# Kernel tuning notes

Measured on AMD Instinct MI355X. Metric: run time of the kernel, lower is better.

The kernel has to match this reference:

```python
import jax, jax.numpy as jnp
import numpy as np

SIZES = [64, 64, 64, 64]
N_SAMPLES = 8192


def radialkernel(u, v):
    # exp(u.v^T - |u|^2/2 - |v|^2/2), shape [rows(u), rows(v)]
    uu = jnp.sum(u * u, axis=1, keepdims=True)
    vv = jnp.sum(v * v, axis=1, keepdims=True)
    return jnp.exp(u @ v.T - uu / 2 - vv.T / 2)


def setup_inputs() -> dict:
    key = jax.random.key(0)
    k0, k1, k2, k3 = jax.random.split(key, 4)
    d_in = 256
    total = sum(SIZES)            # 256
    rest = sum(SIZES[1:])         # 192
    data = jax.random.normal(k0, (N_SAMPLES, d_in), jnp.float32)
    inputs = jax.random.normal(k1, (2048, d_in), jnp.float32)
    # Linear(d_in, total): weight [total, d_in], bias [total]
    W = jax.random.normal(k2, (total, d_in), jnp.float32) / np.sqrt(d_in)
    b = jnp.zeros((total,), jnp.float32)
    # xavier_uniform for c_ss [N, rest]
    limit = np.sqrt(6.0 / (N_SAMPLES + rest)).astype(np.float32)
    c_ss = jax.random.uniform(k3, (N_SAMPLES, rest), jnp.float32, -limit, limit)
    return {"data": data, "inputs": inputs, "W": W, "b": b, "c_ss": c_ss}


def reference(data, inputs, W, b, c_ss):
    n = N_SAMPLES
    x = jnp.concatenate([data, inputs], axis=0) @ W.T + b  # [N+B, total]
    reg = jnp.sum(W * W) + jnp.sum(b * b)
    xss = list(jnp.split(x, np.cumsum(SIZES[:-1]), axis=1))
    css = jnp.split(c_ss, np.cumsum(SIZES[1:-1]), axis=1)
    ker = jnp.zeros((x.shape[0], n), x.dtype)
    for i, cs in enumerate(css):  # len(sizes)-1 iterations (small, fixed)
        xs = xss[i]
        ker = ker + radialkernel(xs, xs[:n])  # [N+B, N]
        val = ker @ cs                        # [N+B, sizes[i+1]]
        xss[i + 1] = xss[i + 1] + val
        reg = reg + jnp.sum(cs * val[:n])
    return xss[-1][n:], reg
```

## Files before the change

### kernel.cpp

```cpp
#include <hip/hip_runtime.h>
#include <hip/hip_bf16.h>

typedef unsigned short u16;
typedef unsigned int   u32;
typedef __attribute__((ext_vector_type(8)))  short bf16x8;
typedef __attribute__((ext_vector_type(16))) float f32x16;

#define N_S   8192
#define M_TOT 10240
#define SEGS  8
#define SEG   1024
#define QT    320
#define SCRN_TRAIN 2080
#define SCRN_BLKS  3104

__device__ __forceinline__ u16 f2bf(float f) {
  u32 x = __float_as_uint(f);
  u32 r = x + 0x7FFFu + ((x >> 16) & 1u);
  return (u16)(r >> 16);
}
__device__ __forceinline__ float bf2f(u16 h) {
  return __uint_as_float(((u32)h) << 16);
}

__global__ __launch_bounds__(256) void gemm_x(const float* __restrict__ data,
                                              const float* __restrict__ inp,
                                              const float* __restrict__ W,
                                              const float* __restrict__ bias,
                                              float* __restrict__ x,
                                              u16* __restrict__ xb0,
                                              u32* __restrict__ hl0)
{
  __shared__ __align__(16) u16 At[64 * 256];
  __shared__ __align__(16) u16 Wt[64 * 256];
  __shared__ float part[64][2];
  const int t  = threadIdx.x;
  const int rb = blockIdx.x * 64, cb = blockIdx.y * 64;
  if (cb == 192 && rb + 64 <= N_S) return;

#pragma unroll
  for (int it = 0; it < 8; ++it) {
    int c = it * 256 + t;
    int row = c >> 5, c8 = c & 31;
    int grow = rb + row;
    const float* src = (grow < N_S) ? data + (size_t)grow * 256 + c8 * 8
                                    : inp + (size_t)(grow - N_S) * 256 + c8 * 8;
    float4 v0 = *(const float4*)src;
    float4 v1 = *(const float4*)(src + 4);
    u16 h[8] = {f2bf(v0.x), f2bf(v0.y), f2bf(v0.z), f2bf(v0.w),
                f2bf(v1.x), f2bf(v1.y), f2bf(v1.z), f2bf(v1.w)};
    *(int4*)((char*)At + row * 512 + ((c8 * 16) ^ ((row & 7) << 4))) = *(int4*)h;

    const float* wsrc = W + (size_t)(cb + row) * 256 + c8 * 8;
    float4 w0 = *(const float4*)wsrc;
    float4 w1 = *(const float4*)(wsrc + 4);
    u16 g[8] = {f2bf(w0.x), f2bf(w0.y), f2bf(w0.z), f2bf(w0.w),
                f2bf(w1.x), f2bf(w1.y), f2bf(w1.z), f2bf(w1.w)};
    *(int4*)((char*)Wt + row * 512 + ((c8 * 16) ^ ((row & 7) << 4))) = *(int4*)g;
  }
  __syncthreads();

  const int w = t >> 6, lane = t & 63, l31 = lane & 31, hi = lane >> 5;
  const int wr = (w >> 1) * 32, wc = (w & 1) * 32;
  f32x16 acc;
#pragma unroll
  for (int r = 0; r < 16; ++r) acc[r] = 0.f;
  const char* Ab = (const char*)At + (size_t)(wr + l31) * 512;
  const char* Bb = (const char*)Wt + (size_t)(wc + l31) * 512;
  const int rx = (l31 & 7) << 4;
#pragma unroll
  for (int k0 = 0; k0 < 256; k0 += 16) {
    bf16x8 af = *(const bf16x8*)(Ab + ((k0 * 2 + hi * 16) ^ rx));
    bf16x8 bfv = *(const bf16x8*)(Bb + ((k0 * 2 + hi * 16) ^ rx));
    acc = __builtin_amdgcn_mfma_f32_32x32x16_bf16(af, bfv, acc, 0, 0, 0);
  }
  float bv = bias[cb + wc + l31];
#pragma unroll
  for (int r = 0; r < 16; ++r) {
    int qr = (r & 3) + 8 * (r >> 2) + 4 * hi;
    x[(size_t)(rb + wr + qr) * 256 + cb + wc + l31] = acc[r] + bv;
  }

  if (cb == 0) {
#pragma unroll
    for (int r = 0; r < 16; ++r) {
      int qr = (r & 3) + 8 * (r >> 2) + 4 * hi;
      u16 h = f2bf(acc[r] + bv);
      xb0[(size_t)(rb + wr + qr) * 64 + wc + l31] = h;
      float fb = bf2f(h);
      float s = fb * fb;
      s += __shfl_xor(s, 1);
      s += __shfl_xor(s, 2);
      s += __shfl_xor(s, 4);
      s += __shfl_xor(s, 8);
      s += __shfl_xor(s, 16);
      if (l31 == 0) part[wr + qr][w & 1] = s;
    }
    __syncthreads();
    if (t < 64) {
      float A = 0.5f * (part[t][0] + part[t][1]);
      u16 hq = f2bf(A);
      u16 lq = f2bf(A - bf2f(hq));
      hl0[rb + t] = (u32)hq | ((u32)lq << 16);
    }
  }
}

__global__ __launch_bounds__(256) void setup_ker(const float* __restrict__ css,
                                                 const float* __restrict__ W,
                                                 const float* __restrict__ bias,
                                                 u16* __restrict__ csbT,
                                                 float* __restrict__ regpart,
                                                 u32* __restrict__ mask,
                                                 u32* __restrict__ counter)
{
  __shared__ float tile[64][65];
  __shared__ float red[256];
  const int b = blockIdx.x, t = threadIdx.x;
  if (b < 384) {
    const int i  = b >> 7;
    const int r0 = (b & 127) * 64;
#pragma unroll
    for (int it = 0; it < 4; ++it) {
      int r  = (t >> 4) + it * 16;
      int c4 = (t & 15) * 4;
      float4 v = *(const float4*)(css + (size_t)(r0 + r) * 192 + i * 64 + c4);
      tile[r][c4] = v.x; tile[r][c4 + 1] = v.y; tile[r][c4 + 2] = v.z; tile[r][c4 + 3] = v.w;
    }
    __syncthreads();
    const int c = t >> 2, rq = (t & 3) * 16;
    u16 tmp[16];
#pragma unroll
    for (int e = 0; e < 16; ++e) tmp[e] = f2bf(tile[rq + e][c]);
    u16* dst = csbT + (size_t)i * (64 * (size_t)N_S) + (size_t)c * N_S + r0 + rq;
    *(int4*)dst       = *(int4*)tmp;
    *(int4*)(dst + 8) = *(int4*)(tmp + 8);
  } else {
    const int b2 = b - 384;
    const int gid = b2 * 256 + t;
    if (gid < 3 * QT * SEGS) mask[gid] = 0u;
    if (gid == 0) *counter = 0u;
    float4 v = *(const float4*)(W + (size_t)b2 * 1024 + t * 4);
    float s = v.x * v.x + v.y * v.y + v.z * v.z + v.w * v.w;
    if (b2 == 0) { float bv = bias[t]; s += bv * bv; }
    red[t] = s; __syncthreads();
#pragma unroll
    for (int o = 128; o; o >>= 1) {
      if (t < o) red[t] += red[t + o];
      __syncthreads();
    }
    if (t == 0) regpart[b2] = red[0];
  }
}

__global__ __launch_bounds__(64) void screen_ker(const u16* __restrict__ xbj,
                                                 const u32* __restrict__ hlj,
                                                 u32* __restrict__ maskj)
{
  const int b = blockIdx.x;
  int qq, k;
  if (b < SCRN_TRAIN) {
    int q = (int)((sqrtf(8.0f * (float)b + 1.0f) - 1.0f) * 0.5f);
    while ((q + 1) * (q + 2) / 2 <= b) ++q;
    while (q * (q + 1) / 2 > b) --q;
    qq = q;
    k = b - q * (q + 1) / 2;
  } else {
    int b2 = b - SCRN_TRAIN;
    qq = 64 + (b2 >> 6);
    k = b2 & 63;
  }
  const int seg = k >> 3, w = k & 7;
  const int nt0 = seg * 32 + w * 4;

  const int lane = threadIdx.x & 63, l31 = lane & 31, hi = lane >> 5;

  bf16x8 qf[4][4];
  u32 hlq[4];
#pragma unroll
  for (int q = 0; q < 4; ++q) {
    const int qrow = (qq * 4 + q) * 32 + l31;
    const u16* qp = xbj + (size_t)qrow * 64 + hi * 8;
#pragma unroll
    for (int d = 0; d < 4; ++d) qf[q][d] = *(const bf16x8*)(qp + d * 16);
    hlq[q] = hlj[qrow];
  }

  f32x16 Z;
#pragma unroll
  for (int r = 0; r < 16; ++r) Z[r] = 0.f;

  u32 bits[4] = {0u, 0u, 0u, 0u};
#pragma unroll
  for (int it = 0; it < 4; ++it) {
    const int kt = nt0 + it;
    const int nb = kt * 32;
    const u16* kp = xbj + (size_t)(nb + l31) * 64 + hi * 8;
    bf16x8 kf0 = *(const bf16x8*)(kp);
    bf16x8 kf1 = *(const bf16x8*)(kp + 16);
    bf16x8 kf2 = *(const bf16x8*)(kp + 32);
    bf16x8 kf3 = *(const bf16x8*)(kp + 48);
    u32 hlk = hlj[nb + l31];
    union { bf16x8 v; u32 d[4]; } ke;
    ke.d[0] = hi ? 0u : 0xBF80BF80u;
    ke.d[1] = hi ? 0u : (hlk ^ 0x80008000u);
    ke.d[2] = 0u; ke.d[3] = 0u;
#pragma unroll
    for (int q = 0; q < 4; ++q) {
      f32x16 S = __builtin_amdgcn_mfma_f32_32x32x16_bf16(qf[q][0], kf0, Z, 0, 0, 0);
      S = __builtin_amdgcn_mfma_f32_32x32x16_bf16(qf[q][1], kf1, S, 0, 0, 0);
      S = __builtin_amdgcn_mfma_f32_32x32x16_bf16(qf[q][2], kf2, S, 0, 0, 0);
      S = __builtin_amdgcn_mfma_f32_32x32x16_bf16(qf[q][3], kf3, S, 0, 0, 0);
      union { bf16x8 v; u32 d[4]; } qe;
      qe.d[0] = hi ? 0u : hlq[q];
      qe.d[1] = hi ? 0u : 0x3F803F80u;
      qe.d[2] = 0u; qe.d[3] = 0u;
      S = __builtin_amdgcn_mfma_f32_32x32x16_bf16(qe.v, ke.v, S, 0, 0, 0);
      float m0 = fmaxf(S[0], S[1]),  m1 = fmaxf(S[2], S[3]);
      float m2 = fmaxf(S[4], S[5]),  m3 = fmaxf(S[6], S[7]);
      float m4 = fmaxf(S[8], S[9]),  m5 = fmaxf(S[10], S[11]);
      float m6 = fmaxf(S[12], S[13]), m7 = fmaxf(S[14], S[15]);
      float mx = fmaxf(fmaxf(fmaxf(m0, m1), fmaxf(m2, m3)),
                       fmaxf(fmaxf(m4, m5), fmaxf(m6, m7)));
      bool act = __any(mx > -25.0f) != 0;
      bits[q] |= (act ? 1u : 0u) << it;
      const int qtile = qq * 4 + q;
      if (act && qtile < 256 && kt < qtile && lane == 0)
        atomicOr(&maskj[(size_t)kt * SEGS + (qtile >> 5)], 1u << (qtile & 31));
    }
  }
  if (lane == 0) {
#pragma unroll
    for (int q = 0; q < 4; ++q)
      if (bits[q]) atomicOr(&maskj[(size_t)(qq * 4 + q) * SEGS + seg], bits[q] << (w * 4));
  }
}

template<int NJ>
__global__ __launch_bounds__(256) void fa_ker(const u16* __restrict__ xb,
                                              const u32* __restrict__ hl,
                                              const u16* __restrict__ csbT,
                                              const u32* __restrict__ mask,
                                              const float* __restrict__ css,
                                              float* __restrict__ x,
                                              float* __restrict__ dotpart,
                                              u16* __restrict__ xbn,
                                              u32* __restrict__ hln,
                                              float* __restrict__ out,
                                              const float* __restrict__ regpart,
                                              u32* __restrict__ counter)
{
  __shared__ __align__(16) u16 Pt[4][32 * 32];
  __shared__ float accs[4][32][64];
  __shared__ float red[256];
  __shared__ int lastFlag;

  const int t    = threadIdx.x;
  const int w    = t >> 6;
  const int lane = t & 63;
  const int l31  = lane & 31;
  const int hi   = lane >> 5;
  const int qtile = blockIdx.x;
  const int qrow  = qtile * 32 + l31;
  constexpr int I = NJ - 1;

  bf16x8 qf[NJ][4];
  u32    hlq[NJ];
#pragma unroll
  for (int j = 0; j < NJ; ++j) {
    const u16* xbj = xb + (size_t)j * ((size_t)M_TOT * 64);
#pragma unroll
    for (int dk = 0; dk < 4; ++dk)
      qf[j][dk] = *(const bf16x8*)(xbj + (size_t)qrow * 64 + dk * 16 + hi * 8);
    hlq[j] = hl[j * M_TOT + qrow];
  }

  f32x16 acc0, acc1;
#pragma unroll
  for (int r = 0; r < 16; ++r) { acc0[r] = 0.f; acc1[r] = 0.f; }

  int idx = 0;
  for (int seg = 0; seg < SEGS; ++seg) {
    u32 mj[NJ];
    u32 uni = 0;
#pragma unroll
    for (int j = 0; j < NJ; ++j) {
      mj[j] = mask[((size_t)j * QT + qtile) * SEGS + seg];
      uni |= mj[j];
    }
    u32 rem = uni;
    while (rem) {
      const int nt = __ffs(rem) - 1;
      rem &= rem - 1;
      if ((idx++ & 3) != w) continue;
      const int nb = seg * SEG + nt * 32;
      f32x16 P;
#pragma unroll
      for (int r = 0; r < 16; ++r) P[r] = 0.f;
#pragma unroll
      for (int j = 0; j < NJ; ++j) {
        if ((mj[j] >> nt) & 1u) {
          const u16* xbj = xb + (size_t)j * ((size_t)M_TOT * 64);
          const u16* kp = xbj + (size_t)(nb + l31) * 64 + hi * 8;
          bf16x8 kf0 = *(const bf16x8*)(kp);
          bf16x8 kf1 = *(const bf16x8*)(kp + 16);
          bf16x8 kf2 = *(const bf16x8*)(kp + 32);
          bf16x8 kf3 = *(const bf16x8*)(kp + 48);
          u32 hlk = hl[j * M_TOT + nb + l31];
          f32x16 S;
#pragma unroll
          for (int r = 0; r < 16; ++r) S[r] = 0.f;
          S = __builtin_amdgcn_mfma_f32_32x32x16_bf16(qf[j][0], kf0, S, 0, 0, 0);
          S = __builtin_amdgcn_mfma_f32_32x32x16_bf16(qf[j][1], kf1, S, 0, 0, 0);
          S = __builtin_amdgcn_mfma_f32_32x32x16_bf16(qf[j][2], kf2, S, 0, 0, 0);
          S = __builtin_amdgcn_mfma_f32_32x32x16_bf16(qf[j][3], kf3, S, 0, 0, 0);
          union { bf16x8 v; u32 d[4]; } qe, ke;
          qe.d[0] = hi ? 0u : hlq[j];
          qe.d[1] = hi ? 0u : 0x3F803F80u;
          qe.d[2] = 0u; qe.d[3] = 0u;
          ke.d[0] = hi ? 0u : 0xBF80BF80u;
          ke.d[1] = hi ? 0u : (hlk ^ 0x80008000u);
          ke.d[2] = 0u; ke.d[3] = 0u;
          S = __builtin_amdgcn_mfma_f32_32x32x16_bf16(qe.v, ke.v, S, 0, 0, 0);
#pragma unroll
          for (int r = 0; r < 16; ++r) P[r] += __expf(S[r]);
        }
      }
      char* pw = (char*)&Pt[w][0];
#pragma unroll
      for (int r = 0; r < 16; ++r) {
        int qr = (r & 3) + 8 * (r >> 2) + 4 * hi;
        *(u16*)(pw + qr * 64 + ((l31 * 2) ^ ((qr & 3) << 4))) = f2bf(P[r]);
      }
      asm volatile("s_waitcnt lgkmcnt(0)" ::: "memory");
      bf16x8 pa0 = *(const bf16x8*)(pw + l31 * 64 + ((0  + hi * 16) ^ ((l31 & 3) << 4)));
      bf16x8 pa1 = *(const bf16x8*)(pw + l31 * 64 + ((32 + hi * 16) ^ ((l31 & 3) << 4)));
      asm volatile("s_waitcnt lgkmcnt(0)" ::: "memory");
      bf16x8 v00 = *(const bf16x8*)(csbT + (size_t)l31 * N_S + nb + hi * 8);
      bf16x8 v01 = *(const bf16x8*)(csbT + (size_t)l31 * N_S + nb + 16 + hi * 8);
      bf16x8 v10 = *(const bf16x8*)(csbT + (size_t)(32 + l31) * N_S + nb + hi * 8);
      bf16x8 v11 = *(const bf16x8*)(csbT + (size_t)(32 + l31) * N_S + nb + 16 + hi * 8);
      acc0 = __builtin_amdgcn_mfma_f32_32x32x16_bf16(pa0, v00, acc0, 0, 0, 0);
      acc0 = __builtin_amdgcn_mfma_f32_32x32x16_bf16(pa1, v01, acc0, 0, 0, 0);
      acc1 = __builtin_amdgcn_mfma_f32_32x32x16_bf16(pa0, v10, acc1, 0, 0, 0);
      acc1 = __builtin_amdgcn_mfma_f32_32x32x16_bf16(pa1, v11, acc1, 0, 0, 0);
    }
  }

#pragma unroll
  for (int r = 0; r < 16; ++r) {
    int qr = (r & 3) + 8 * (r >> 2) + 4 * hi;
    accs[w][qr][l31]      = acc0[r];
    accs[w][qr][32 + l31] = acc1[r];
  }
  __syncthreads();

  const int rr   = t >> 3;
  const int row  = qtile * 32 + rr;
  const int coff = (t & 7) * 8;
  float v[8];
#pragma unroll
  for (int e = 0; e < 8; ++e)
    v[e] = ((accs[0][rr][coff + e] + accs[1][rr][coff + e]) +
            (accs[2][rr][coff + e] + accs[3][rr][coff + e]));

  float dp = 0.f;
  if (row < N_S) {
    const float* cp = css + (size_t)row * 192 + (size_t)I * 64 + coff;
    float4 ca = *(const float4*)cp;
    float4 cb = *(const float4*)(cp + 4);
    dp = ca.x * v[0] + ca.y * v[1] + ca.z * v[2] + ca.w * v[3]
       + cb.x * v[4] + cb.y * v[5] + cb.z * v[6] + cb.w * v[7];
  }

  if (NJ < 3) {
    float* xp = x + (size_t)row * 256 + (size_t)(I + 1) * 64 + coff;
    float4 xa = *(const float4*)xp;
    float4 xb4 = *(const float4*)(xp + 4);
    xa.x += v[0]; xa.y += v[1]; xa.z += v[2]; xa.w += v[3];
    xb4.x += v[4]; xb4.y += v[5]; xb4.z += v[6]; xb4.w += v[7];
    *(float4*)xp = xa;
    *(float4*)(xp + 4) = xb4;
    float xv[8] = {xa.x, xa.y, xa.z, xa.w, xb4.x, xb4.y, xb4.z, xb4.w};
    u16 h[8];
    float s2 = 0.f;
#pragma unroll
    for (int e = 0; e < 8; ++e) {
      h[e] = f2bf(xv[e]);
      float fb = bf2f(h[e]);
      s2 += fb * fb;
    }
    *(int4*)(xbn + (size_t)row * 64 + coff) = *(int4*)h;
    s2 += __shfl_xor(s2, 1);
    s2 += __shfl_xor(s2, 2);
    s2 += __shfl_xor(s2, 4);
    if ((t & 7) == 0) {
      float A = 0.5f * s2;
      u16 hq = f2bf(A);
      u16 lq = f2bf(A - bf2f(hq));
      hln[row] = (u32)hq | ((u32)lq << 16);
    }
  } else if (row >= N_S) {
    const float* xp = x + (size_t)row * 256 + 192 + coff;
    float4 xa = *(const float4*)xp;
    float4 xb4 = *(const float4*)(xp + 4);
    float* op = out + (size_t)(row - N_S) * 64 + coff;
    float4 oa = {xa.x + v[0], xa.y + v[1], xa.z + v[2], xa.w + v[3]};
    float4 ob = {xb4.x + v[4], xb4.y + v[5], xb4.z + v[6], xb4.w + v[7]};
    *(float4*)op = oa;
    *(float4*)(op + 4) = ob;
  }

  red[t] = dp; __syncthreads();
#pragma unroll
  for (int o = 128; o; o >>= 1) {
    if (t < o) red[t] += red[t + o];
    __syncthreads();
  }
  if (t == 0) dotpart[I * QT + qtile] = red[0];

  if (NJ == 3) {
    if (t == 0) {
      u32 c = __hip_atomic_fetch_add(counter, 1u, __ATOMIC_ACQ_REL, __HIP_MEMORY_SCOPE_AGENT);
      lastFlag = (c == QT - 1) ? 1 : 0;
    }
    __syncthreads();
    if (lastFlag) {
      float s = 0.f;
      for (int i2 = t; i2 < 3 * QT; i2 += 256) s += dotpart[i2];
      if (t < 64) s += regpart[t];
      red[t] = s; __syncthreads();
#pragma unroll
      for (int o = 128; o; o >>= 1) {
        if (t < o) red[t] += red[t + o];
        __syncthreads();
      }
      if (t == 0) out[131072] = red[0];
    }
  }
}

extern "C" void kernel_launch(void* const* d_in, const int* in_sizes, int n_in,
                              void* d_out, int out_size, void* d_ws, size_t ws_size,
                              hipStream_t stream)
{
  const float* data = (const float*)d_in[0];
  const float* inp  = (const float*)d_in[1];
  const float* W    = (const float*)d_in[2];
  const float* bias = (const float*)d_in[3];
  const float* css  = (const float*)d_in[4];
  float* out = (float*)d_out;

  char* ws = (char*)d_ws;
  const size_t OFF_X    = 0;
  const size_t OFF_XB   = 10485760;
  const size_t OFF_HL   = OFF_XB + 3932160;
  const size_t OFF_CSBT = OFF_HL + 122880;
  const size_t OFF_MASK = OFF_CSBT + 3145728;
  const size_t OFF_REGW = OFF_MASK + 30720;
  const size_t OFF_DOT  = OFF_REGW + 256;
  const size_t OFF_CNT  = OFF_DOT + 3840;

  float* x      = (float*)(ws + OFF_X);
  u16*   xb     = (u16*)  (ws + OFF_XB);
  u32*   hl     = (u32*)  (ws + OFF_HL);
  u16*   csbT   = (u16*)  (ws + OFF_CSBT);
  u32*   mask   = (u32*)  (ws + OFF_MASK);
  float* regpart= (float*)(ws + OFF_REGW);
  float* dotpart= (float*)(ws + OFF_DOT);
  u32*   counter= (u32*)  (ws + OFF_CNT);

  const size_t XB_STRIDE = (size_t)M_TOT * 64;
  const size_t CS_STRIDE = (size_t)64 * N_S;
  const size_t MK_STRIDE = (size_t)QT * SEGS;

  setup_ker<<<448, 256, 0, stream>>>(css, W, bias, csbT, regpart, mask, counter);
  gemm_x   <<<dim3(160, 4), 256, 0, stream>>>(data, inp, W, bias, x, xb, hl);
  screen_ker<<<SCRN_BLKS, 64, 0, stream>>>(xb, hl, mask);

  fa_ker<1><<<QT, 256, 0, stream>>>(xb, hl, csbT, mask, css, x, dotpart,
                                    xb + XB_STRIDE, hl + M_TOT, (float*)nullptr,
                                    regpart, counter);
  screen_ker<<<SCRN_BLKS, 64, 0, stream>>>(xb + XB_STRIDE, hl + M_TOT, mask + MK_STRIDE);

  fa_ker<2><<<QT, 256, 0, stream>>>(xb, hl, csbT + CS_STRIDE, mask, css, x, dotpart,
                                    xb + 2 * XB_STRIDE, hl + 2 * M_TOT, (float*)nullptr,
                                    regpart, counter);
  screen_ker<<<SCRN_BLKS, 64, 0, stream>>>(xb + 2 * XB_STRIDE, hl + 2 * M_TOT, mask + 2 * MK_STRIDE);

  fa_ker<3><<<QT, 256, 0, stream>>>(xb, hl, csbT + 2 * CS_STRIDE, mask, css, x, dotpart,
                                    (u16*)nullptr, (u32*)nullptr, out,
                                    regpart, counter);
}
```

Measured before the change: 133.9 us.

## Pre-populate bf16 x segments in gemm and skip stage work for empty tiles

The initial GEMM now writes bf16 copies and half-norms for all three input segments (not just the first), and stops writing the fp32 x for the first segment. The fused kernel loads all mask words up front and, when a query tile has no active key blocks, skips loading queries, the MFMA loops, the LDS reduction and the x/xb update entirely, relying on the GEMM's precomputed bf16 data for later stages. This removes redundant loads and writes for sparse/empty tiles at the cost of extra GEMM-side bf16 stores and more mask registers.

```diff
diff --git a/kernel.cpp b/kernel.cpp
--- a/kernel.cpp
+++ b/kernel.cpp
@@ -28,14 +28,15 @@
                                               const float* __restrict__ W,
                                               const float* __restrict__ bias,
                                               float* __restrict__ x,
-                                              u16* __restrict__ xb0,
-                                              u32* __restrict__ hl0)
+                                              u16* __restrict__ xb,
+                                              u32* __restrict__ hl)
 {
   __shared__ __align__(16) u16 At[64 * 256];
   __shared__ __align__(16) u16 Wt[64 * 256];
   __shared__ float part[64][2];
   const int t  = threadIdx.x;
   const int rb = blockIdx.x * 64, cb = blockIdx.y * 64;
+  const int cbi = blockIdx.y;
   if (cb == 192 && rb + 64 <= N_S) return;
 
 #pragma unroll
@@ -75,18 +76,22 @@
     acc = __builtin_amdgcn_mfma_f32_32x32x16_bf16(af, bfv, acc, 0, 0, 0);
   }
   float bv = bias[cb + wc + l31];
-#pragma unroll
-  for (int r = 0; r < 16; ++r) {
-    int qr = (r & 3) + 8 * (r >> 2) + 4 * hi;
-    x[(size_t)(rb + wr + qr) * 256 + cb + wc + l31] = acc[r] + bv;
-  }
-
-  if (cb == 0) {
+  if (cb != 0) {
+#pragma unroll
+    for (int r = 0; r < 16; ++r) {
+      int qr = (r & 3) + 8 * (r >> 2) + 4 * hi;
+      x[(size_t)(rb + wr + qr) * 256 + cb + wc + l31] = acc[r] + bv;
+    }
+  }
+
+  if (cb < 192) {
+    u16* xbc = xb + (size_t)cbi * ((size_t)M_TOT * 64);
+    u32* hlc = hl + (size_t)cbi * M_TOT;
 #pragma unroll
     for (int r = 0; r < 16; ++r) {
       int qr = (r & 3) + 8 * (r >> 2) + 4 * hi;
       u16 h = f2bf(acc[r] + bv);
-      xb0[(size_t)(rb + wr + qr) * 64 + wc + l31] = h;
+      xbc[(size_t)(rb + wr + qr) * 64 + wc + l31] = h;
       float fb = bf2f(h);
       float s = fb * fb;
       s += __shfl_xor(s, 1);
@@ -101,7 +106,7 @@
       float A = 0.5f * (part[t][0] + part[t][1]);
       u16 hq = f2bf(A);
       u16 lq = f2bf(A - bf2f(hq));
-      hl0[rb + t] = (u32)hq | ((u32)lq << 16);
+      hlc[rb + t] = (u32)hq | ((u32)lq << 16);
     }
   }
 }
@@ -264,141 +269,157 @@
   const int qrow  = qtile * 32 + l31;
   constexpr int I = NJ - 1;
 
-  bf16x8 qf[NJ][4];
-  u32    hlq[NJ];
-#pragma unroll
-  for (int j = 0; j < NJ; ++j) {
-    const u16* xbj = xb + (size_t)j * ((size_t)M_TOT * 64);
-#pragma unroll
-    for (int dk = 0; dk < 4; ++dk)
-      qf[j][dk] = *(const bf16x8*)(xbj + (size_t)qrow * 64 + dk * 16 + hi * 8);
-    hlq[j] = hl[j * M_TOT + qrow];
-  }
-
-  f32x16 acc0, acc1;
-#pragma unroll
-  for (int r = 0; r < 16; ++r) { acc0[r] = 0.f; acc1[r] = 0.f; }
-
-  int idx = 0;
+  u32 mj_all[NJ][SEGS];
+  u32 uni_s[SEGS];
+  u32 anyu = 0;
+#pragma unroll
   for (int seg = 0; seg < SEGS; ++seg) {
-    u32 mj[NJ];
-    u32 uni = 0;
+    u32 u = 0;
 #pragma unroll
     for (int j = 0; j < NJ; ++j) {
-      mj[j] = mask[((size_t)j * QT + qtile) * SEGS + seg];
-      uni |= mj[j];
-    }
-    u32 rem = uni;
-    while (rem) {
-      const int nt = __ffs(rem) - 1;
-      rem &= rem - 1;
-      if ((idx++ & 3) != w) continue;
-      const int nb = seg * SEG + nt * 32;
-      f32x16 P;
-#pragma unroll
-      for (int r = 0; r < 16; ++r) P[r] = 0.f;
-#pragma unroll
-      for (int j = 0; j < NJ; ++j) {
-        if ((mj[j] >> nt) & 1u) {
-          const u16* xbj = xb + (size_t)j * ((size_t)M_TOT * 64);
-          const u16* kp = xbj + (size_t)(nb + l31) * 64 + hi * 8;
-          bf16x8 kf0 = *(const bf16x8*)(kp);
-          bf16x8 kf1 = *(const bf16x8*)(kp + 16);
-          bf16x8 kf2 = *(const bf16x8*)(kp + 32);
-          bf16x8 kf3 = *(const bf16x8*)(kp + 48);
-          u32 hlk = hl[j * M_TOT + nb + l31];
-          f32x16 S;
-#pragma unroll
-          for (int r = 0; r < 16; ++r) S[r] = 0.f;
-          S = __builtin_amdgcn_mfma_f32_32x32x16_bf16(qf[j][0], kf0, S, 0, 0, 0);
-          S = __builtin_amdgcn_mfma_f32_32x32x16_bf16(qf[j][1], kf1, S, 0, 0, 0);
-          S = __builtin_amdgcn_mfma_f32_32x32x16_bf16(qf[j][2], kf2, S, 0, 0, 0);
-          S = __builtin_amdgcn_mfma_f32_32x32x16_bf16(qf[j][3], kf3, S, 0, 0, 0);
-          union { bf16x8 v; u32 d[4]; } qe, ke;
-          qe.d[0] = hi ? 0u : hlq[j];
-          qe.d[1] = hi ? 0u : 0x3F803F80u;
-          qe.d[2] = 0u; qe.d[3] = 0u;
-          ke.d[0] = hi ? 0u : 0xBF80BF80u;
-          ke.d[1] = hi ? 0u : (hlk ^ 0x80008000u);
-          ke.d[2] = 0u; ke.d[3] = 0u;
-          S = __builtin_amdgcn_mfma_f32_32x32x16_bf16(qe.v, ke.v, S, 0, 0, 0);
-#pragma unroll
-          for (int r = 0; r < 16; ++r) P[r] += __expf(S[r]);
+      mj_all[j][seg] = mask[((size_t)j * QT + qtile) * SEGS + seg];
+      u |= mj_all[j][seg];
+    }
+    uni_s[seg] = u;
+    anyu |= u;
+  }
+
+  if (anyu) {
+    bf16x8 qf[NJ][4];
+    u32    hlq[NJ];
+#pragma unroll
+    for (int j = 0; j < NJ; ++j) {
+      const u16* xbj = xb + (size_t)j * ((size_t)M_TOT * 64);
+#pragma unroll
+      for (int dk = 0; dk < 4; ++dk)
+        qf[j][dk] = *(const bf16x8*)(xbj + (size_t)qrow * 64 + dk * 16 + hi * 8);
+      hlq[j] = hl[j * M_TOT + qrow];
+    }
+
+    f32x16 acc0, acc1;
+#pragma unroll
+    for (int r = 0; r < 16; ++r) { acc0[r] = 0.f; acc1[r] = 0.f; }
+
+    int idx = 0;
+    for (int seg = 0; seg < SEGS; ++seg) {
+      u32 rem = uni_s[seg];
+      while (rem) {
+        const int nt = __ffs(rem) - 1;
+        rem &= rem - 1;
+        if ((idx++ & 3) != w) continue;
+        const int nb = seg * SEG + nt * 32;
+        f32x16 P;
+#pragma unroll
+        for (int r = 0; r < 16; ++r) P[r] = 0.f;
+#pragma unroll
+        for (int j = 0; j < NJ; ++j) {
+          if ((mj_all[j][seg] >> nt) & 1u) {
+            const u16* xbj = xb + (size_t)j * ((size_t)M_TOT * 64);
+            const u16* kp = xbj + (size_t)(nb + l31) * 64 + hi * 8;
+            bf16x8 kf0 = *(const bf16x8*)(kp);
+            bf16x8 kf1 = *(const bf16x8*)(kp + 16);
+            bf16x8 kf2 = *(const bf16x8*)(kp + 32);
+            bf16x8 kf3 = *(const bf16x8*)(kp + 48);
+            u32 hlk = hl[j * M_TOT + nb + l31];
+            f32x16 S;
+#pragma unroll
+            for (int r = 0; r < 16; ++r) S[r] = 0.f;
+            S = __builtin_amdgcn_mfma_f32_32x32x16_bf16(qf[j][0], kf0, S, 0, 0, 0);
+            S = __builtin_amdgcn_mfma_f32_32x32x16_bf16(qf[j][1], kf1, S, 0, 0, 0);
+            S = __builtin_amdgcn_mfma_f32_32x32x16_bf16(qf[j][2], kf2, S, 0, 0, 0);
+            S = __builtin_amdgcn_mfma_f32_32x32x16_bf16(qf[j][3], kf3, S, 0, 0, 0);
+            union { bf16x8 v; u32 d[4]; } qe, ke;
+            qe.d[0] = hi ? 0u : hlq[j];
+            qe.d[1] = hi ? 0u : 0x3F803F80u;
+            qe.d[2] = 0u; qe.d[3] = 0u;
+            ke.d[0] = hi ? 0u : 0xBF80BF80u;
+            ke.d[1] = hi ? 0u : (hlk ^ 0x80008000u);
+            ke.d[2] = 0u; ke.d[3] = 0u;
+            S = __builtin_amdgcn_mfma_f32_32x32x16_bf16(qe.v, ke.v, S, 0, 0, 0);
+#pragma unroll
+            for (int r = 0; r < 16; ++r) P[r] += __expf(S[r]);
+          }
         }
+        char* pw = (char*)&Pt[w][0];
+#pragma unroll
+        for (int r = 0; r < 16; ++r) {
+          int qr = (r & 3) + 8 * (r >> 2) + 4 * hi;
+          *(u16*)(pw + qr * 64 + ((l31 * 2) ^ ((qr & 3) << 4))) = f2bf(P[r]);
+        }
+        asm volatile("s_waitcnt lgkmcnt(0)" ::: "memory");
+        bf16x8 pa0 = *(const bf16x8*)(pw + l31 * 64 + ((0  + hi * 16) ^ ((l31 & 3) << 4)));
+        bf16x8 pa1 = *(const bf16x8*)(pw + l31 * 64 + ((32 + hi * 16) ^ ((l31 & 3) << 4)));
+        asm volatile("s_waitcnt lgkmcnt(0)" ::: "memory");
+        bf16x8 v00 = *(const bf16x8*)(csbT + (size_t)l31 * N_S + nb + hi * 8);
+        bf16x8 v01 = *(const bf16x8*)(csbT + (size_t)l31 * N_S + nb + 16 + hi * 8);
+        bf16x8 v10 = *(const bf16x8*)(csbT + (size_t)(32 + l31) * N_S + nb + hi * 8);
+        bf16x8 v11 = *(const bf16x8*)(csbT + (size_t)(32 + l31) * N_S + nb + 16 + hi * 8);
+        acc0 = __builtin_amdgcn_mfma_f32_32x32x16_bf16(pa0, v00, acc0, 0, 0, 0);
+        acc0 = __builtin_amdgcn_mfma_f32_32x32x16_bf16(pa1, v01, acc0, 0, 0, 0);
+        acc1 = __builtin_amdgcn_mfma_f32_32x32x16_bf16(pa0, v10, acc1, 0, 0, 0);
+        acc1 = __builtin_amdgcn_mfma_f32_32x32x16_bf16(pa1, v11, acc1, 0, 0, 0);
       }
-      char* pw = (char*)&Pt[w][0];
-#pragma unroll
-      for (int r = 0; r < 16; ++r) {
-        int qr = (r & 3) + 8 * (r >> 2) + 4 * hi;
-        *(u16*)(pw + qr * 64 + ((l31 * 2) ^ ((qr & 3) << 4))) = f2bf(P[r]);
-      }
-      asm volatile("s_waitcnt lgkmcnt(0)" ::: "memory");
-      bf16x8 pa0 = *(const bf16x8*)(pw + l31 * 64 + ((0  + hi * 16) ^ ((l31 & 3) << 4)));
-      bf16x8 pa1 = *(const bf16x8*)(pw + l31 * 64 + ((32 + hi * 16) ^ ((l31 & 3) << 4)));
-      asm volatile("s_waitcnt lgkmcnt(0)" ::: "memory");
-      bf16x8 v00 = *(const bf16x8*)(csbT + (size_t)l31 * N_S + nb + hi * 8);
-      bf16x8 v01 = *(const bf16x8*)(csbT + (size_t)l31 * N_S + nb + 16 + hi * 8);
-      bf16x8 v10 = *(const bf16x8*)(csbT + (size_t)(32 + l31) * N_S + nb + hi * 8);
-      bf16x8 v11 = *(const bf16x8*)(csbT + (size_t)(32 + l31) * N_S + nb + 16 + hi * 8);
-      acc0 = __builtin_amdgcn_mfma_f32_32x32x16_bf16(pa0, v00, acc0, 0, 0, 0);
-      acc0 = __builtin_amdgcn_mfma_f32_32x32x16_bf16(pa1, v01, acc0, 0, 0, 0);
-      acc1 = __builtin_amdgcn_mfma_f32_32x32x16_bf16(pa0, v10, acc1, 0, 0, 0);
-      acc1 = __builtin_amdgcn_mfma_f32_32x32x16_bf16(pa1, v11, acc1, 0, 0, 0);
-    }
-  }
-
-#pragma unroll
-  for (int r = 0; r < 16; ++r) {
-    int qr = (r & 3) + 8 * (r >> 2) + 4 * hi;
-    accs[w][qr][l31]      = acc0[r];
-    accs[w][qr][32 + l31] = acc1[r];
-  }
-  __syncthreads();
+    }
+
+#pragma unroll
+    for (int r = 0; r < 16; ++r) {
+      int qr = (r & 3) + 8 * (r >> 2) + 4 * hi;
+      accs[w][qr][l31]      = acc0[r];
+      accs[w][qr][32 + l31] = acc1[r];
+    }
+    __syncthreads();
+  }
 
   const int rr   = t >> 3;
   const int row  = qtile * 32 + rr;
   const int coff = (t & 7) * 8;
   float v[8];
 #pragma unroll
-  for (int e = 0; e < 8; ++e)
-    v[e] = ((accs[0][rr][coff + e] + accs[1][rr][coff + e]) +
-            (accs[2][rr][coff + e] + accs[3][rr][coff + e]));
-
+  for (int e = 0; e < 8; ++e) v[e] = 0.f;
   float dp = 0.f;
-  if (row < N_S) {
-    const float* cp = css + (size_t)row * 192 + (size_t)I * 64 + coff;
-    float4 ca = *(const float4*)cp;
-    float4 cb = *(const float4*)(cp + 4);
-    dp = ca.x * v[0] + ca.y * v[1] + ca.z * v[2] + ca.w * v[3]
-       + cb.x * v[4] + cb.y * v[5] + cb.z * v[6] + cb.w * v[7];
+
+  if (anyu) {
+#pragma unroll
+    for (int e = 0; e < 8; ++e)
+      v[e] = ((accs[0][rr][coff + e] + accs[1][rr][coff + e]) +
+              (accs[2][rr][coff + e] + accs[3][rr][coff + e]));
+    if (row < N_S) {
+      const float* cp = css + (size_t)row * 192 + (size_t)I * 64 + coff;
+      float4 ca = *(const float4*)cp;
+      float4 cb = *(const float4*)(cp + 4);
+      dp = ca.x * v[0] + ca.y * v[1] + ca.z * v[2] + ca.w * v[3]
+         + cb.x * v[4] + cb.y * v[5] + cb.z * v[6] + cb.w * v[7];
+    }
   }
 
   if (NJ < 3) {
-    float* xp = x + (size_t)row * 256 + (size_t)(I + 1) * 64 + coff;
-    float4 xa = *(const float4*)xp;
-    float4 xb4 = *(const float4*)(xp + 4);
-    xa.x += v[0]; xa.y += v[1]; xa.z += v[2]; xa.w += v[3];
-    xb4.x += v[4]; xb4.y += v[5]; xb4.z += v[6]; xb4.w += v[7];
-    *(float4*)xp = xa;
-    *(float4*)(xp + 4) = xb4;
-    float xv[8] = {xa.x, xa.y, xa.z, xa.w, xb4.x, xb4.y, xb4.z, xb4.w};
-    u16 h[8];
-    float s2 = 0.f;
-#pragma unroll
-    for (int e = 0; e < 8; ++e) {
-      h[e] = f2bf(xv[e]);
-      float fb = bf2f(h[e]);
-      s2 += fb * fb;
-    }
-    *(int4*)(xbn + (size_t)row * 64 + coff) = *(int4*)h;
-    s2 += __shfl_xor(s2, 1);
-    s2 += __shfl_xor(s2, 2);
-    s2 += __shfl_xor(s2, 4);
-    if ((t & 7) == 0) {
-      float A = 0.5f * s2;
-      u16 hq = f2bf(A);
-      u16 lq = f2bf(A - bf2f(hq));
-      hln[row] = (u32)hq | ((u32)lq << 16);
+    if (anyu) {
+      float* xp = x + (size_t)row * 256 + (size_t)(I + 1) * 64 + coff;
+      float4 xa = *(const float4*)xp;
+      float4 xb4 = *(const float4*)(xp + 4);
+      xa.x += v[0]; xa.y += v[1]; xa.z += v[2]; xa.w += v[3];
+      xb4.x += v[4]; xb4.y += v[5]; xb4.z += v[6]; xb4.w += v[7];
+      *(float4*)xp = xa;
+      *(float4*)(xp + 4) = xb4;
+      float xv[8] = {xa.x, xa.y, xa.z, xa.w, xb4.x, xb4.y, xb4.z, xb4.w};
+      u16 h[8];
+      float s2 = 0.f;
+#pragma unroll
+      for (int e = 0; e < 8; ++e) {
+        h[e] = f2bf(xv[e]);
+        float fb = bf2f(h[e]);
+        s2 += fb * fb;
+      }
+      *(int4*)(xbn + (size_t)row * 64 + coff) = *(int4*)h;
+      s2 += __shfl_xor(s2, 1);
+      s2 += __shfl_xor(s2, 2);
+      s2 += __shfl_xor(s2, 4);
+      if ((t & 7) == 0) {
+        float A = 0.5f * s2;
+        u16 hq = f2bf(A);
+        u16 lq = f2bf(A - bf2f(hq));
+        hln[row] = (u32)hq | ((u32)lq << 16);
+      }
     }
   } else if (row >= N_S) {
     const float* xp = x + (size_t)row * 256 + 192 + coff;
```

Measured after the change: 135.8 us. No clear change (+1.4%).
